# Performance work log

Measured on AMD Instinct MI355X. Metric: run time of the kernel, lower is better.

## Reference

```python
import jax, jax.numpy as jnp
import numpy as np

B, S, D = 32, 512, 512
H, DK, DV, DFF = 8, 64, 64, 2048
TEMP = float(np.sqrt(DK))  # d_k ** 0.5
COS_EPS = 1e-8             # torch.cosine_similarity eps
LN_EPS = 1e-5


def _layernorm(x, g, b):
    mu = jnp.mean(x, axis=-1, keepdims=True)
    var = jnp.var(x, axis=-1, keepdims=True)
    return (x - mu) * jax.lax.rsqrt(var + LN_EPS) * g + b


def setup_inputs() -> dict:
    key = jax.random.key(0)
    ks = jax.random.split(key, 12)
    s = 0.02
    return {
        "x": jax.random.normal(ks[0], (B, S, D), dtype=jnp.float32),
        "w_q": jax.random.normal(ks[1], (D, H * DK), dtype=jnp.float32) * s,
        "w_k": jax.random.normal(ks[2], (D, H * DK), dtype=jnp.float32) * s,
        "w_v": jax.random.normal(ks[3], (D, H * DV), dtype=jnp.float32) * s,
        "w_o": jax.random.normal(ks[4], (H * DV, D), dtype=jnp.float32) * s,
        "w_ff1": jax.random.normal(ks[5], (D, DFF), dtype=jnp.float32) * s,
        "b_ff1": jnp.zeros((DFF,), dtype=jnp.float32),
        "w_ff2": jax.random.normal(ks[6], (DFF, D), dtype=jnp.float32) * s,
        "b_ff2": jnp.zeros((D,), dtype=jnp.float32),
        "g1": jnp.ones((D,), dtype=jnp.float32),
        "b1": jnp.zeros((D,), dtype=jnp.float32),
        "g2": jnp.ones((D,), dtype=jnp.float32),
        "b2": jnp.zeros((D,), dtype=jnp.float32),
    }


def reference(x, w_q, w_k, w_v, w_o, w_ff1, b_ff1, w_ff2, b_ff2, g1, b1, g2, b2):
    b, s, _ = x.shape
    # projections -> [b, h, s, d]
    q = (x @ w_q).reshape(b, s, H, DK).transpose(0, 2, 1, 3)
    k = (x @ w_k).reshape(b, s, H, DK).transpose(0, 2, 1, 3)
    v = (x @ w_v).reshape(b, s, H, DV).transpose(0, 2, 1, 3)
    # cosine-similarity attention: dot(q,k) / max(||q||*||k||, eps) / temperature
    scores = jnp.einsum("bhqd,bhkd->bhqk", q, k)
    nq = jnp.linalg.norm(q, axis=-1)  # [b,h,s]
    nk = jnp.linalg.norm(k, axis=-1)
    denom = jnp.maximum(nq[:, :, :, None] * nk[:, :, None, :], COS_EPS)
    attn = jax.nn.softmax(scores / denom / TEMP, axis=-1)
    out = jnp.einsum("bhqk,bhkd->bhqd", attn, v)  # [b,h,s,dv]
    out = out.transpose(0, 2, 1, 3).reshape(b, s, H * DV) @ w_o
    # residual + LN1
    h1 = _layernorm(x + out, g1, b1)
    # FFN
    ffn = jax.nn.relu(h1 @ w_ff1 + b_ff1) @ w_ff2 + b_ff2
    # residual + LN2
    return _layernorm(h1 + ffn, g2, b2)
```

## Files before the change

### kernel.cpp

```cpp
#include <hip/hip_runtime.h>
#include <cmath>

typedef __bf16 bf16x8 __attribute__((ext_vector_type(8)));
typedef __bf16 bf16x4 __attribute__((ext_vector_type(4)));
typedef float  floatx4 __attribute__((ext_vector_type(4)));

#define LN_EPS 1e-5f
#define INV_TEMP 0.125f

static const int Mrows = 16384;

__device__ __forceinline__ void gload_lds16(const void* g, void* l) {
  __builtin_amdgcn_global_load_lds(
      (const __attribute__((address_space(1))) void*)g,
      (__attribute__((address_space(3))) void*)l, 16, 0, 0);
}

__global__ __launch_bounds__(256) void prep_kernel(const float* __restrict__ x, __bf16* __restrict__ xb,
                                                   const float* __restrict__ wq, const float* __restrict__ wk,
                                                   const float* __restrict__ wv, const float* __restrict__ wo,
                                                   const float* __restrict__ wff1, const float* __restrict__ wff2,
                                                   __bf16* __restrict__ tq, __bf16* __restrict__ tk,
                                                   __bf16* __restrict__ tv, __bf16* __restrict__ to_,
                                                   __bf16* __restrict__ tff1, __bf16* __restrict__ tff2) {
  const int bid = blockIdx.x, tid = threadIdx.x;
  if (bid < 8192) {
    int i = bid * 256 + tid;
    float4 v = ((const float4*)x)[i];
    __bf16* d = xb + i * 4;
    d[0] = (__bf16)v.x; d[1] = (__bf16)v.y; d[2] = (__bf16)v.z; d[3] = (__bf16)v.w;
    return;
  }
  __shared__ __bf16 til[64][72];
  int t = bid - 8192;
  const float* src; __bf16* dst; int R, C, bx, by;
  if (t < 256) {
    int w = t >> 6, tt = t & 63;
    const float* srcs[4] = {wq, wk, wv, wo};
    __bf16* dsts[4] = {tq, tk, tv, to_};
    src = srcs[w]; dst = dsts[w]; R = 512; C = 512; bx = tt & 7; by = tt >> 3;
  } else if (t < 512) {
    int tt = t - 256;
    src = wff1; dst = tff1; R = 512; C = 2048; bx = tt & 31; by = tt >> 5;
  } else {
    int tt = t - 512;
    src = wff2; dst = tff2; R = 2048; C = 512; bx = tt & 7; by = tt >> 3;
  }
  const float* s = src + (size_t)(by * 64) * C + bx * 64;
  int r = tid >> 4, c4 = (tid & 15) * 4;
  for (int p = 0; p < 4; ++p) {
    int rr = r + p * 16;
    float4 v = *(const float4*)(s + (size_t)rr * C + c4);
    til[c4 + 0][rr] = (__bf16)v.x;
    til[c4 + 1][rr] = (__bf16)v.y;
    til[c4 + 2][rr] = (__bf16)v.z;
    til[c4 + 3][rr] = (__bf16)v.w;
  }
  __syncthreads();
  __bf16* d = dst + (size_t)(bx * 64) * R + by * 64;
  int orow = tid >> 3, oc8 = (tid & 7) * 8;
  for (int p = 0; p < 2; ++p) {
    int rr = orow + p * 32;
    *(bf16x8*)(d + (size_t)rr * R + oc8) = *(const bf16x8*)(&til[rr][oc8]);
  }
}

template <int EPI, int NBN, int NDIM, int KDIM>
__global__ __launch_bounds__(256) void gemm_bt(const __bf16* __restrict__ A,
                                               const __bf16* __restrict__ Bt,
                                               __bf16* __restrict__ Cv,
                                               const float* __restrict__ bias,
                                               float* __restrict__ norms,
                                               __bf16* __restrict__ vtg) {
  __shared__ __align__(16) char smem[128 * 144 * 2];
  __bf16* As = (__bf16*)smem;
  __bf16* Bs = (__bf16*)(smem + 16384);
  const int tid = threadIdx.x;
  const int wave = tid >> 6, lane = tid & 63;
  const int l15 = lane & 15, quad = lane >> 4;
  const int id = blockIdx.x;
  const int xcd = id & 7, t = id >> 3;
  const int nblk = t % NBN, mblk = (t / NBN) * 8 + xcd;
  const int m0 = mblk * 128, n0 = nblk * 128;
  const int wrow = (wave >> 1) * 64, wcol = (wave & 1) * 64;
  const int rs = lane >> 3;
  const int swz_st = ((lane & 7) ^ rs) * 8;
  const int s7 = l15 & 7;

  floatx4 zero = {0.f, 0.f, 0.f, 0.f};
  floatx4 acc[4][4];
  for (int i = 0; i < 4; ++i)
    for (int j = 0; j < 4; ++j) acc[i][j] = zero;

  for (int kt = 0; kt < KDIM; kt += 64) {
    __syncthreads();
    for (int c = 0; c < 8; ++c) {
      int g = wave * 8 + c;
      const __bf16* src;
      __bf16* dst;
      if (g < 16) {
        int row = m0 + g * 8 + rs;
        src = A + (size_t)row * KDIM + kt + swz_st;
        dst = As + g * 512;
      } else {
        int g2 = g - 16;
        int row = n0 + g2 * 8 + rs;
        src = Bt + (size_t)row * KDIM + kt + swz_st;
        dst = Bs + g2 * 512;
      }
      gload_lds16(src, dst + lane * 8);
    }
    __syncthreads();
    for (int hh = 0; hh < 2; ++hh) {
      int ko = ((hh * 4 + quad) ^ s7) * 8;
      bf16x8 a[4], b[4];
      for (int i = 0; i < 4; ++i)
        a[i] = *(const bf16x8*)(As + (wrow + i * 16 + l15) * 64 + ko);
      for (int j = 0; j < 4; ++j)
        b[j] = *(const bf16x8*)(Bs + (wcol + j * 16 + l15) * 64 + ko);
      for (int i = 0; i < 4; ++i)
        for (int j = 0; j < 4; ++j)
          acc[i][j] = __builtin_amdgcn_mfma_f32_16x16x32_bf16(a[i], b[j], acc[i][j], 0, 0, 0);
    }
  }

  if (EPI == 4) {
    int head_global = (n0 + wcol) >> 6;
    int kind = head_global >> 3;
    if (kind < 2) {
      int h = head_global & 7;
      for (int i = 0; i < 4; ++i)
        for (int r = 0; r < 4; ++r) {
          float sq = 0.f;
          for (int j = 0; j < 4; ++j) {
            float v = acc[i][j][r];
            sq += v * v;
          }
          for (int m = 1; m < 16; m <<= 1) sq += __shfl_xor(sq, m, 64);
          if (l15 == 0) {
            int arow = m0 + wrow + i * 16 + quad * 4 + r;
            int bb = arow >> 9, ss = arow & 511;
            norms[kind * 131072 + ((bb << 3) + h) * 512 + ss] = rsqrtf(sq);
          }
        }
    } else {
      __syncthreads();
      __bf16* Ct = (__bf16*)smem;
      for (int i = 0; i < 4; ++i)
        for (int j = 0; j < 4; ++j) {
          bf16x4 pk;
          for (int r = 0; r < 4; ++r) pk[r] = (__bf16)acc[i][j][r];
          *(bf16x4*)(Ct + (wcol + j * 16 + l15) * 136 + wrow + i * 16 + quad * 4) = pk;
        }
      __syncthreads();
      int b = mblk >> 2, s0r = (mblk & 3) * 128;
      for (int p = 0; p < 8; ++p) {
        int row = p * 16 + (tid >> 4);
        int c8 = (tid & 15) * 8;
        int colg = n0 + row;
        int h = (colg >> 6) & 7, d = colg & 63;
        *(bf16x8*)(vtg + ((size_t)(((b << 3) + h) * 64 + d)) * 512 + s0r + c8) =
            *(const bf16x8*)(Ct + row * 136 + c8);
      }
      return;
    }
  }

  __syncthreads();
  __bf16* Cs = (__bf16*)smem;
  for (int i = 0; i < 4; ++i)
    for (int j = 0; j < 4; ++j) {
      int coll = wcol + j * 16 + l15;
      float bv = (EPI == 2) ? bias[n0 + coll] : 0.f;
      for (int r = 0; r < 4; ++r) {
        float v = acc[i][j][r];
        if (EPI == 2) {
          v += bv;
          v = v > 0.f ? v : 0.f;
        }
        Cs[(wrow + i * 16 + quad * 4 + r) * 144 + coll] = (__bf16)v;
      }
    }
  __syncthreads();
  for (int p = 0; p < 8; ++p) {
    int row = p * 16 + (tid >> 4);
    int c8 = (tid & 15) * 8;
    *(bf16x8*)(Cv + (size_t)(m0 + row) * NDIM + n0 + c8) =
        *(const bf16x8*)(Cs + row * 144 + c8);
  }
}

template <int EPI, int NBN, int NDIM, int KDIM, int NKS>
__global__ __launch_bounds__(512, 2) void gemm256(const __bf16* __restrict__ A,
                                                  const __bf16* __restrict__ Bt,
                                                  __bf16* __restrict__ Cv,
                                                  const float* __restrict__ bias) {
  __shared__ __align__(16) char smem[131072];
  const int tid = threadIdx.x;
  const int wave = tid >> 6, lane = tid & 63;
  const int l15 = lane & 15, quad = lane >> 4;
  const int wm = wave >> 2, wn = wave & 3;
  const int s7 = l15 & 7;
  const int rs = lane >> 3, slot = lane & 7;
  const int swz = (slot ^ rs) * 8;

  constexpr int NBM = Mrows / 256;
  constexpr int NBLK = NBM * NBN * NKS;
  constexpr int KS = KDIM / NKS;
  constexpr int NT = KS / 64;

  int id = blockIdx.x;
  int t = (id & 7) * (NBLK >> 3) + (id >> 3);
  const int ks = t / (NBM * NBN);
  t -= ks * (NBM * NBN);
  const int nblk = t % NBN, mblk = t / NBN;
  const int m0 = mblk * 256, n0 = nblk * 256;
  const __bf16* Ab = A + (size_t)ks * KS;
  const __bf16* Bb = Bt + (size_t)ks * KS;
  __bf16* Cw = Cv + (size_t)ks * Mrows * NDIM;
  (void)bias;

  const __bf16* sb[4][2];
  int ldo[4][2];
#pragma unroll
  for (int s = 0; s < 4; ++s)
#pragma unroll
    for (int j = 0; j < 2; ++j) {
      int chunk;
      if (s < 2) {
        int c = (wave & 3) * 4 + s * 2 + j;
        if (wave < 4) chunk = (c < 8) ? c : c + 8;
        else          chunk = 32 + ((c >> 2) * 8 + (c & 3));
      } else if (s == 2) {
        int c = 2 * wave + j;
        chunk = (c < 8) ? c + 8 : c + 16;
      } else {
        int c = 2 * wave + j;
        chunk = 32 + ((c >> 2) * 8 + 4 + (c & 3));
      }
      int isB = chunk >= 32 ? 1 : 0;
      int cc = chunk - isB * 32;
      int row = cc * 8 + rs;
      sb[s][j] = (isB ? (Bb + (size_t)(n0 + row) * KDIM)
                      : (Ab + (size_t)(m0 + row) * KDIM)) + swz;
      ldo[s][j] = isB * 32768 + cc * 1024 + lane * 16;
    }

  floatx4 zero = {0.f, 0.f, 0.f, 0.f};
  floatx4 acc[8][4];
#pragma unroll
  for (int i = 0; i < 8; ++i)
#pragma unroll
    for (int j = 0; j < 4; ++j) acc[i][j] = zero;

#define STAGE256(s, ktel, bufb)                                              \
  {                                                                          \
    gload_lds16(sb[s][0] + (ktel), smem + (bufb) * 65536 + ldo[s][0]);       \
    gload_lds16(sb[s][1] + (ktel), smem + (bufb) * 65536 + ldo[s][1]);       \
  }

#define PHASE256(q, ia, jb, bufb, DOSTAGE, ktel)                                   \
  {                                                                                \
    const __bf16* Abuf = (const __bf16*)(smem + (bufb) * 65536);                   \
    const __bf16* Bbuf = Abuf + 16384;                                             \
    bf16x8 af[4][2], bfr[2][2];                                                    \
    _Pragma("unroll") for (int i = 0; i < 4; ++i) {                                \
      int row = wm * 128 + (ia) * 64 + i * 16 + l15;                               \
      af[i][0] = *(const bf16x8*)(Abuf + row * 64 + ((quad ^ s7) * 8));            \
      af[i][1] = *(const bf16x8*)(Abuf + row * 64 + (((4 + quad) ^ s7) * 8));      \
    }                                                                              \
    _Pragma("unroll") for (int j = 0; j < 2; ++j) {                                \
      int row = wn * 64 + (jb) * 32 + j * 16 + l15;                                \
      bfr[j][0] = *(const bf16x8*)(Bbuf + row * 64 + ((quad ^ s7) * 8));           \
      bfr[j][1] = *(const bf16x8*)(Bbuf + row * 64 + (((4 + quad) ^ s7) * 8));     \
    }                                                                              \
    if (DOSTAGE) STAGE256(q, ktel, (bufb) ^ 1);                                    \
    __builtin_amdgcn_s_barrier();                                                  \
    asm volatile("s_waitcnt lgkmcnt(0)" ::: "memory");                             \
    __builtin_amdgcn_s_setprio(1);                                                 \
    _Pragma("unroll") for (int i = 0; i < 4; ++i)                                  \
      _Pragma("unroll") for (int j = 0; j < 2; ++j) {                              \
        acc[(ia) * 4 + i][(jb) * 2 + j] = __builtin_amdgcn_mfma_f32_16x16x32_bf16( \
            af[i][0], bfr[j][0], acc[(ia) * 4 + i][(jb) * 2 + j], 0, 0, 0);        \
        acc[(ia) * 4 + i][(jb) * 2 + j] = __builtin_amdgcn_mfma_f32_16x16x32_bf16( \
            af[i][1], bfr[j][1], acc[(ia) * 4 + i][(jb) * 2 + j], 0, 0, 0);        \
      }                                                                            \
    __builtin_amdgcn_s_setprio(0);                                                 \
    asm volatile("s_waitcnt vmcnt(4)" ::: "memory");                               \
    __builtin_amdgcn_s_barrier();                                                  \
  }

#pragma unroll
  for (int s = 0; s < 4; ++s) STAGE256(s, 0, 0);
  asm volatile("s_waitcnt vmcnt(0)" ::: "memory");
  __builtin_amdgcn_s_barrier();

  for (int t2 = 0; t2 < NT - 1; ++t2) {
    int b = t2 & 1;
    int k1 = (t2 + 1) * 64;
    PHASE256(0, 0, 0, b, 1, k1);
    PHASE256(1, 1, 0, b, 1, k1);
    PHASE256(2, 1, 1, b, 1, k1);
    PHASE256(3, 0, 1, b, 1, k1);
  }
  asm volatile("s_waitcnt vmcnt(0)" ::: "memory");
  __builtin_amdgcn_s_barrier();
  {
    const int b = (NT - 1) & 1;
    PHASE256(0, 0, 0, b, 0, 0);
    PHASE256(1, 1, 0, b, 0, 0);
    PHASE256(2, 1, 1, b, 0, 0);
    PHASE256(3, 0, 1, b, 0, 0);
  }

  const int PADC = 264;
  __bf16* Cs = (__bf16*)smem;
  float bv[4];
  if (EPI == 2) {
#pragma unroll
    for (int j = 0; j < 4; ++j) bv[j] = bias[n0 + wn * 64 + j * 16 + l15];
  }
#pragma unroll
  for (int hh = 0; hh < 2; ++hh) {
    __builtin_amdgcn_s_barrier();
    if (wm == hh) {
#pragma unroll
      for (int i = 0; i < 8; ++i)
#pragma unroll
        for (int j = 0; j < 4; ++j)
#pragma unroll
          for (int r = 0; r < 4; ++r) {
            float v = acc[i][j][r];
            if (EPI == 2) {
              v += bv[j];
              v = v > 0.f ? v : 0.f;
            }
            Cs[(i * 16 + quad * 4 + r) * PADC + wn * 64 + j * 16 + l15] = (__bf16)v;
          }
    }
    __builtin_amdgcn_s_barrier();
#pragma unroll
    for (int p = 0; p < 8; ++p) {
      int rowl = p * 16 + (tid >> 5);
      int c8 = (tid & 31) * 8;
      *(bf16x8*)(Cw + (size_t)(m0 + hh * 128 + rowl) * NDIM + n0 + c8) =
          *(const bf16x8*)(Cs + rowl * PADC + c8);
    }
  }
#undef STAGE256
#undef PHASE256
}

__global__ __launch_bounds__(256) void attn_kernel(const __bf16* __restrict__ qkv,
                                                   const __bf16* __restrict__ vtg,
                                                   const float* __restrict__ norms,
                                                   __bf16* __restrict__ out) {
  __shared__ __align__(16) __bf16 Ks[64 * 64];
  __shared__ __align__(16) __bf16 Vs[64 * 64];
  __shared__ __align__(16) __bf16 P2[4][16 * 72];
  const int tid = threadIdx.x, wave = tid >> 6, lane = tid & 63;
  const int l15 = lane & 15, quad = lane >> 4;
  const int bh = blockIdx.x & 255;
  const int qq = blockIdx.x >> 8;
  const int b = bh >> 3, h = bh & 7;
  const int qbase = qq * 128 + wave * 32;
  const int rs = lane >> 3;
  const int swz_st = ((lane & 7) ^ rs) * 8;
  const int s7 = l15 & 7;

  const __bf16* Qb = qkv + (size_t)(b * 512) * 1536 + h * 64;
  const __bf16* Kb = Qb + 512;
  const __bf16* Vtb = vtg + (size_t)bh * 32768;
  const float* nkinv = norms + 131072 + bh * 512;
  const float* nqinv = norms + bh * 512;
  __bf16* Pw = P2[wave];

  bf16x8 aq[2][2];
  float cq[2];
  for (int ch = 0; ch < 2; ++ch) {
    int qrow = qbase + ch * 16;
    aq[ch][0] = *(const bf16x8*)(Qb + (size_t)(qrow + l15) * 1536 + quad * 8);
    aq[ch][1] = *(const bf16x8*)(Qb + (size_t)(qrow + l15) * 1536 + 32 + quad * 8);
    cq[ch] = nqinv[qrow + l15] * INV_TEMP;
  }

  floatx4 zero = {0.f, 0.f, 0.f, 0.f};
  floatx4 o[2][4];
  float lsum[2] = {0.f, 0.f};
  for (int ch = 0; ch < 2; ++ch)
    for (int jd = 0; jd < 4; ++jd) o[ch][jd] = zero;

  for (int kt = 0; kt < 8; ++kt) {
    int s0 = kt * 64;
    __syncthreads();
    for (int c = 0; c < 4; ++c) {
      int g = wave * 4 + c;
      const __bf16* src;
      __bf16* dst;
      if (g < 8) {
        int sk = g * 8 + rs;
        src = Kb + (size_t)(s0 + sk) * 1536 + swz_st;
        dst = Ks + g * 512;
      } else {
        int g2 = g - 8;
        int d = g2 * 8 + rs;
        src = Vtb + (size_t)d * 512 + s0 + swz_st;
        dst = Vs + g2 * 512;
      }
      gload_lds16(src, dst + lane * 8);
    }
    __syncthreads();

    for (int ch = 0; ch < 2; ++ch) {
      floatx4 z[4];
      for (int j = 0; j < 4; ++j) {
        int r64 = (j * 16 + l15) * 64;
        bf16x8 k0 = *(const bf16x8*)(Ks + r64 + ((quad ^ s7) * 8));
        bf16x8 k1 = *(const bf16x8*)(Ks + r64 + (((4 + quad) ^ s7) * 8));
        floatx4 zz = zero;
        zz = __builtin_amdgcn_mfma_f32_16x16x32_bf16(k0, aq[ch][0], zz, 0, 0, 0);
        zz = __builtin_amdgcn_mfma_f32_16x16x32_bf16(k1, aq[ch][1], zz, 0, 0, 0);
        z[j] = zz;
      }
      for (int j = 0; j < 4; ++j) {
        floatx4 nk4 = *(const floatx4*)(nkinv + s0 + j * 16 + quad * 4);
        bf16x4 pk;
        for (int r = 0; r < 4; ++r) {
          float p = __expf(z[j][r] * cq[ch] * nk4[r]);
          lsum[ch] += p;
          pk[r] = (__bf16)p;
        }
        *(bf16x4*)(Pw + l15 * 72 + j * 16 + quad * 4) = pk;
      }
      bf16x8 ap0 = *(const bf16x8*)(Pw + l15 * 72 + quad * 8);
      bf16x8 ap1 = *(const bf16x8*)(Pw + l15 * 72 + 32 + quad * 8);
      for (int jd = 0; jd < 4; ++jd) {
        int r64 = (jd * 16 + l15) * 64;
        bf16x8 v0 = *(const bf16x8*)(Vs + r64 + ((quad ^ s7) * 8));
        bf16x8 v1 = *(const bf16x8*)(Vs + r64 + (((4 + quad) ^ s7) * 8));
        o[ch][jd] = __builtin_amdgcn_mfma_f32_16x16x32_bf16(v0, ap0, o[ch][jd], 0, 0, 0);
        o[ch][jd] = __builtin_amdgcn_mfma_f32_16x16x32_bf16(v1, ap1, o[ch][jd], 0, 0, 0);
      }
    }
  }

  for (int ch = 0; ch < 2; ++ch) {
    float s = lsum[ch];
    s += __shfl_xor(s, 16, 64);
    s += __shfl_xor(s, 32, 64);
    float inv = __builtin_amdgcn_rcpf(s);
    int q = qbase + ch * 16 + l15;
    __bf16* op = out + (size_t)(b * 512 + q) * 512 + h * 64;
    for (int jd = 0; jd < 4; ++jd) {
      bf16x4 pk;
      for (int r = 0; r < 4; ++r) pk[r] = (__bf16)(o[ch][jd][r] * inv);
      *(bf16x4*)(op + jd * 16 + quad * 4) = pk;
    }
  }
}

template <bool X1BF, bool WF, bool WB, bool DUAL>
__global__ __launch_bounds__(256) void resid_ln(const float* __restrict__ X1f,
                                                const __bf16* __restrict__ X1b,
                                                const __bf16* __restrict__ X2,
                                                const __bf16* __restrict__ X2b,
                                                const float* __restrict__ bias,
                                                const float* __restrict__ g,
                                                const float* __restrict__ be,
                                                float* __restrict__ outf,
                                                __bf16* __restrict__ outb) {
  int row = blockIdx.x * 4 + (threadIdx.x >> 6);
  int lane = threadIdx.x & 63;
  float v[8];
  bf16x8 b8 = *(const bf16x8*)(X2 + (size_t)row * 512 + lane * 8);
  if (X1BF) {
    bf16x8 a = *(const bf16x8*)(X1b + (size_t)row * 512 + lane * 8);
    for (int i = 0; i < 8; ++i) v[i] = (float)a[i] + (float)b8[i];
  } else {
    const float4* r1 = (const float4*)(X1f + (size_t)row * 512);
    float4 a0 = r1[lane * 2], a1 = r1[lane * 2 + 1];
    v[0] = a0.x; v[1] = a0.y; v[2] = a0.z; v[3] = a0.w;
    v[4] = a1.x; v[5] = a1.y; v[6] = a1.z; v[7] = a1.w;
    for (int i = 0; i < 8; ++i) v[i] += (float)b8[i];
  }
  if (DUAL) {
    bf16x8 c8 = *(const bf16x8*)(X2b + (size_t)row * 512 + lane * 8);
    for (int i = 0; i < 8; ++i) v[i] += (float)c8[i];
  }
  if (bias) {
    const float* bp = bias + lane * 8;
    for (int i = 0; i < 8; ++i) v[i] += bp[i];
  }
  float s = 0.f, sq = 0.f;
  for (int i = 0; i < 8; ++i) {
    s += v[i];
    sq += v[i] * v[i];
  }
  for (int m = 1; m < 64; m <<= 1) {
    s += __shfl_xor(s, m, 64);
    sq += __shfl_xor(sq, m, 64);
  }
  float mean = s * (1.f / 512.f);
  float var = sq * (1.f / 512.f) - mean * mean;
  float rstd = rsqrtf(var + LN_EPS);
  const float* gp = g + lane * 8;
  const float* bp2 = be + lane * 8;
  float o[8];
  for (int i = 0; i < 8; ++i) o[i] = (v[i] - mean) * rstd * gp[i] + bp2[i];
  if (WF) {
    float4 w0 = {o[0], o[1], o[2], o[3]}, w1 = {o[4], o[5], o[6], o[7]};
    ((float4*)(outf + (size_t)row * 512))[lane * 2] = w0;
    ((float4*)(outf + (size_t)row * 512))[lane * 2 + 1] = w1;
  }
  if (WB) {
    __bf16 tmp[8];
    for (int i = 0; i < 8; ++i) tmp[i] = (__bf16)o[i];
    *(bf16x8*)(outb + (size_t)row * 512 + lane * 8) = *(bf16x8*)tmp;
  }
}

extern "C" void kernel_launch(void* const* d_in, const int* in_sizes, int n_in,
                              void* d_out, int out_size, void* d_ws, size_t ws_size,
                              hipStream_t stream) {
  const float* x     = (const float*)d_in[0];
  const float* w_q   = (const float*)d_in[1];
  const float* w_k   = (const float*)d_in[2];
  const float* w_v   = (const float*)d_in[3];
  const float* w_o   = (const float*)d_in[4];
  const float* w_ff1 = (const float*)d_in[5];
  const float* b_ff1 = (const float*)d_in[6];
  const float* w_ff2 = (const float*)d_in[7];
  const float* b_ff2 = (const float*)d_in[8];
  const float* g1    = (const float*)d_in[9];
  const float* b1    = (const float*)d_in[10];
  const float* g2    = (const float*)d_in[11];
  const float* b2    = (const float*)d_in[12];
  float* out = (float*)d_out;

  char* ws = (char*)d_ws;
  size_t off = 0;
  auto alloc = [&](size_t bytes) -> void* {
    void* p = ws + off;
    off += (bytes + 255) & ~(size_t)255;
    return p;
  };
  __bf16* xb     = (__bf16*)alloc((size_t)Mrows * 512 * 2);
  __bf16* wt_qkv = (__bf16*)alloc((size_t)1536 * 512 * 2);
  __bf16* wt_o   = (__bf16*)alloc((size_t)512 * 512 * 2);
  __bf16* wt_ff1 = (__bf16*)alloc((size_t)2048 * 512 * 2);
  __bf16* wt_ff2 = (__bf16*)alloc((size_t)512 * 2048 * 2);
  __bf16* qkv    = (__bf16*)alloc((size_t)Mrows * 1536 * 2);
  float*  norms  = (float*)alloc((size_t)262144 * 4);
  __bf16* attn   = (__bf16*)alloc((size_t)Mrows * 512 * 2);
  __bf16* projb  = (__bf16*)alloc((size_t)Mrows * 512 * 2);
  __bf16* h1b    = (__bf16*)alloc((size_t)Mrows * 512 * 2);
  __bf16* mid    = (__bf16*)alloc((size_t)Mrows * 2048 * 2);
  __bf16* vtg    = mid;
  __bf16* f2o    = attn;

  prep_kernel<<<8960, 256, 0, stream>>>(x, xb, w_q, w_k, w_v, w_o, w_ff1, w_ff2,
                                        wt_qkv, wt_qkv + 512 * 512, wt_qkv + 2 * 512 * 512,
                                        wt_o, wt_ff1, wt_ff2);

  gemm_bt<4, 12, 1536, 512><<<dim3(12 * 128), 256, 0, stream>>>(xb, wt_qkv, qkv, nullptr,
                                                                norms, vtg);
  attn_kernel<<<dim3(1024), 256, 0, stream>>>(qkv, vtg, norms, attn);
  gemm_bt<0, 4, 512, 512><<<dim3(4 * 128), 256, 0, stream>>>(attn, wt_o, projb, nullptr,
                                                             nullptr, nullptr);
  resid_ln<false, false, true, false><<<4096, 256, 0, stream>>>(x, nullptr, projb, nullptr,
                                                                nullptr, g1, b1, nullptr, h1b);
  gemm256<2, 8, 2048, 512, 1><<<dim3(512), 512, 0, stream>>>(h1b, wt_ff1, mid, b_ff1);
  gemm256<0, 2, 512, 2048, 2><<<dim3(256), 512, 0, stream>>>(mid, wt_ff2, f2o, nullptr);
  resid_ln<true, true, false, true><<<4096, 256, 0, stream>>>(nullptr, h1b, f2o,
                                                              f2o + (size_t)Mrows * 512,
                                                              b_ff2, g2, b2, out, nullptr);
}
```

Before: 320.9 us.

## Move QKV projection to 256x256 gemm with fused norm/V-transpose epilogue and reworked pipeline

The QKV projection now runs on the 256x256-tile, 512-thread gemm256 kernel instead of the 128-tile gemm_bt. The norm and V-transpose epilogue is moved into gemm256 so the larger tile still produces the cosine norms and the transposed V. The gemm256 main loop is also restructured: each wave stages contiguous rows, and a k-tile is split into four MFMA quadrants with A/B fragment loads interleaved between barriers. This aims for more reuse per block and better overlap of LDS reads with MFMA. The cost is more barriers per k-tile and a full vmcnt(0) wait at the end of each tile, and the changes also affect the FF1 and FF2 gemms.

```diff
diff --git a/kernel.cpp b/kernel.cpp
--- a/kernel.cpp
+++ b/kernel.cpp
@@ -124,48 +124,6 @@
     }
   }
 
-  if (EPI == 4) {
-    int head_global = (n0 + wcol) >> 6;
-    int kind = head_global >> 3;
-    if (kind < 2) {
-      int h = head_global & 7;
-      for (int i = 0; i < 4; ++i)
-        for (int r = 0; r < 4; ++r) {
-          float sq = 0.f;
-          for (int j = 0; j < 4; ++j) {
-            float v = acc[i][j][r];
-            sq += v * v;
-          }
-          for (int m = 1; m < 16; m <<= 1) sq += __shfl_xor(sq, m, 64);
-          if (l15 == 0) {
-            int arow = m0 + wrow + i * 16 + quad * 4 + r;
-            int bb = arow >> 9, ss = arow & 511;
-            norms[kind * 131072 + ((bb << 3) + h) * 512 + ss] = rsqrtf(sq);
-          }
-        }
-    } else {
-      __syncthreads();
-      __bf16* Ct = (__bf16*)smem;
-      for (int i = 0; i < 4; ++i)
-        for (int j = 0; j < 4; ++j) {
-          bf16x4 pk;
-          for (int r = 0; r < 4; ++r) pk[r] = (__bf16)acc[i][j][r];
-          *(bf16x4*)(Ct + (wcol + j * 16 + l15) * 136 + wrow + i * 16 + quad * 4) = pk;
-        }
-      __syncthreads();
-      int b = mblk >> 2, s0r = (mblk & 3) * 128;
-      for (int p = 0; p < 8; ++p) {
-        int row = p * 16 + (tid >> 4);
-        int c8 = (tid & 15) * 8;
-        int colg = n0 + row;
-        int h = (colg >> 6) & 7, d = colg & 63;
-        *(bf16x8*)(vtg + ((size_t)(((b << 3) + h) * 64 + d)) * 512 + s0r + c8) =
-            *(const bf16x8*)(Ct + row * 136 + c8);
-      }
-      return;
-    }
-  }
-
   __syncthreads();
   __bf16* Cs = (__bf16*)smem;
   for (int i = 0; i < 4; ++i)
@@ -194,7 +152,9 @@
 __global__ __launch_bounds__(512, 2) void gemm256(const __bf16* __restrict__ A,
                                                   const __bf16* __restrict__ Bt,
                                                   __bf16* __restrict__ Cv,
-                                                  const float* __restrict__ bias) {
+                                                  const float* __restrict__ bias,
+                                                  float* __restrict__ norms,
+                                                  __bf16* __restrict__ vtg) {
   __shared__ __align__(16) char smem[131072];
   const int tid = threadIdx.x;
   const int wave = tid >> 6, lane = tid & 63;
@@ -220,31 +180,12 @@
   __bf16* Cw = Cv + (size_t)ks * Mrows * NDIM;
   (void)bias;
 
-  const __bf16* sb[4][2];
-  int ldo[4][2];
-#pragma unroll
-  for (int s = 0; s < 4; ++s)
-#pragma unroll
-    for (int j = 0; j < 2; ++j) {
-      int chunk;
-      if (s < 2) {
-        int c = (wave & 3) * 4 + s * 2 + j;
-        if (wave < 4) chunk = (c < 8) ? c : c + 8;
-        else          chunk = 32 + ((c >> 2) * 8 + (c & 3));
-      } else if (s == 2) {
-        int c = 2 * wave + j;
-        chunk = (c < 8) ? c + 8 : c + 16;
-      } else {
-        int c = 2 * wave + j;
-        chunk = 32 + ((c >> 2) * 8 + 4 + (c & 3));
-      }
-      int isB = chunk >= 32 ? 1 : 0;
-      int cc = chunk - isB * 32;
-      int row = cc * 8 + rs;
-      sb[s][j] = (isB ? (Bb + (size_t)(n0 + row) * KDIM)
-                      : (Ab + (size_t)(m0 + row) * KDIM)) + swz;
-      ldo[s][j] = isB * 32768 + cc * 1024 + lane * 16;
-    }
+  const int isB = wave >= 4 ? 1 : 0;
+  const int w3 = wave & 3;
+  const __bf16* sbase = isB
+      ? Bb + (size_t)(n0 + w3 * 64 + rs) * KDIM + swz
+      : Ab + (size_t)(m0 + w3 * 64 + rs) * KDIM + swz;
+  const int ldob = isB * 32768 + w3 * 8192 + lane * 16;
 
   floatx4 zero = {0.f, 0.f, 0.f, 0.f};
   floatx4 acc[8][4];
@@ -253,64 +194,145 @@
 #pragma unroll
     for (int j = 0; j < 4; ++j) acc[i][j] = zero;
 
-#define STAGE256(s, ktel, bufb)                                              \
-  {                                                                          \
-    gload_lds16(sb[s][0] + (ktel), smem + (bufb) * 65536 + ldo[s][0]);       \
-    gload_lds16(sb[s][1] + (ktel), smem + (bufb) * 65536 + ldo[s][1]);       \
-  }
-
-#define PHASE256(q, ia, jb, bufb, DOSTAGE, ktel)                                   \
+  bf16x8 aR[4][2];
+  bf16x8 bC[2][2][2];
+
+#define STAGE8(jj, ktel, bufb)                                             \
+  gload_lds16(sbase + (size_t)(jj) * (8 * KDIM) + (ktel),                  \
+              smem + (bufb) * 65536 + ldob + (jj) * 1024);
+
+#define LDA256(ia, bufb)                                                        \
+  {                                                                             \
+    const __bf16* Abuf = (const __bf16*)(smem + (size_t)(bufb) * 65536);        \
+    _Pragma("unroll") for (int i = 0; i < 4; ++i) {                             \
+      int row = wm * 128 + (ia) * 64 + i * 16 + l15;                            \
+      aR[i][0] = *(const bf16x8*)(Abuf + row * 64 + ((quad ^ s7) * 8));         \
+      aR[i][1] = *(const bf16x8*)(Abuf + row * 64 + (((4 + quad) ^ s7) * 8));   \
+    }                                                                           \
+  }
+
+#define LDB256(jb, bufb)                                                              \
+  {                                                                                   \
+    const __bf16* Bbuf = (const __bf16*)(smem + (size_t)(bufb) * 65536) + 16384;      \
+    _Pragma("unroll") for (int j = 0; j < 2; ++j) {                                   \
+      int row = wn * 64 + (jb) * 32 + j * 16 + l15;                                   \
+      bC[jb][j][0] = *(const bf16x8*)(Bbuf + row * 64 + ((quad ^ s7) * 8));           \
+      bC[jb][j][1] = *(const bf16x8*)(Bbuf + row * 64 + (((4 + quad) ^ s7) * 8));     \
+    }                                                                                 \
+  }
+
+#define MFMAQ(ia, jb)                                                              \
   {                                                                                \
-    const __bf16* Abuf = (const __bf16*)(smem + (bufb) * 65536);                   \
-    const __bf16* Bbuf = Abuf + 16384;                                             \
-    bf16x8 af[4][2], bfr[2][2];                                                    \
-    _Pragma("unroll") for (int i = 0; i < 4; ++i) {                                \
-      int row = wm * 128 + (ia) * 64 + i * 16 + l15;                               \
-      af[i][0] = *(const bf16x8*)(Abuf + row * 64 + ((quad ^ s7) * 8));            \
-      af[i][1] = *(const bf16x8*)(Abuf + row * 64 + (((4 + quad) ^ s7) * 8));      \
-    }                                                                              \
-    _Pragma("unroll") for (int j = 0; j < 2; ++j) {                                \
-      int row = wn * 64 + (jb) * 32 + j * 16 + l15;                                \
-      bfr[j][0] = *(const bf16x8*)(Bbuf + row * 64 + ((quad ^ s7) * 8));           \
-      bfr[j][1] = *(const bf16x8*)(Bbuf + row * 64 + (((4 + quad) ^ s7) * 8));     \
-    }                                                                              \
-    if (DOSTAGE) STAGE256(q, ktel, (bufb) ^ 1);                                    \
-    __builtin_amdgcn_s_barrier();                                                  \
-    asm volatile("s_waitcnt lgkmcnt(0)" ::: "memory");                             \
     __builtin_amdgcn_s_setprio(1);                                                 \
     _Pragma("unroll") for (int i = 0; i < 4; ++i)                                  \
       _Pragma("unroll") for (int j = 0; j < 2; ++j) {                              \
         acc[(ia) * 4 + i][(jb) * 2 + j] = __builtin_amdgcn_mfma_f32_16x16x32_bf16( \
-            af[i][0], bfr[j][0], acc[(ia) * 4 + i][(jb) * 2 + j], 0, 0, 0);        \
+            aR[i][0], bC[jb][j][0], acc[(ia) * 4 + i][(jb) * 2 + j], 0, 0, 0);     \
         acc[(ia) * 4 + i][(jb) * 2 + j] = __builtin_amdgcn_mfma_f32_16x16x32_bf16( \
-            af[i][1], bfr[j][1], acc[(ia) * 4 + i][(jb) * 2 + j], 0, 0, 0);        \
+            aR[i][1], bC[jb][j][1], acc[(ia) * 4 + i][(jb) * 2 + j], 0, 0, 0);     \
       }                                                                            \
     __builtin_amdgcn_s_setprio(0);                                                 \
-    asm volatile("s_waitcnt vmcnt(4)" ::: "memory");                               \
-    __builtin_amdgcn_s_barrier();                                                  \
-  }
-
-#pragma unroll
-  for (int s = 0; s < 4; ++s) STAGE256(s, 0, 0);
+  }
+
+#define KTILE(bufb, DOSTAGE, ktel)                                         \
+  {                                                                        \
+    LDA256(0, bufb);                                                       \
+    LDB256(0, bufb);                                                       \
+    if (DOSTAGE) {                                                         \
+      STAGE8(0, ktel, (bufb) ^ 1); STAGE8(1, ktel, (bufb) ^ 1);            \
+      STAGE8(2, ktel, (bufb) ^ 1); STAGE8(3, ktel, (bufb) ^ 1);            \
+    }                                                                      \
+    __builtin_amdgcn_s_barrier();                                          \
+    asm volatile("s_waitcnt lgkmcnt(0)" ::: "memory");                     \
+    MFMAQ(0, 0);                                                           \
+    __builtin_amdgcn_s_barrier();                                          \
+    LDB256(1, bufb);                                                       \
+    if (DOSTAGE) {                                                         \
+      STAGE8(4, ktel, (bufb) ^ 1); STAGE8(5, ktel, (bufb) ^ 1);            \
+      STAGE8(6, ktel, (bufb) ^ 1); STAGE8(7, ktel, (bufb) ^ 1);            \
+    }                                                                      \
+    __builtin_amdgcn_s_barrier();                                          \
+    asm volatile("s_waitcnt lgkmcnt(0)" ::: "memory");                     \
+    MFMAQ(0, 1);                                                           \
+    __builtin_amdgcn_s_barrier();                                          \
+    LDA256(1, bufb);                                                       \
+    __builtin_amdgcn_s_barrier();                                          \
+    asm volatile("s_waitcnt lgkmcnt(0)" ::: "memory");                     \
+    MFMAQ(1, 1);                                                           \
+    __builtin_amdgcn_s_barrier();                                          \
+    MFMAQ(1, 0);                                                           \
+    if (DOSTAGE) asm volatile("s_waitcnt vmcnt(0)" ::: "memory");          \
+    __builtin_amdgcn_s_barrier();                                          \
+  }
+
+#pragma unroll
+  for (int jj = 0; jj < 8; ++jj) STAGE8(jj, 0, 0);
   asm volatile("s_waitcnt vmcnt(0)" ::: "memory");
   __builtin_amdgcn_s_barrier();
 
   for (int t2 = 0; t2 < NT - 1; ++t2) {
-    int b = t2 & 1;
-    int k1 = (t2 + 1) * 64;
-    PHASE256(0, 0, 0, b, 1, k1);
-    PHASE256(1, 1, 0, b, 1, k1);
-    PHASE256(2, 1, 1, b, 1, k1);
-    PHASE256(3, 0, 1, b, 1, k1);
-  }
-  asm volatile("s_waitcnt vmcnt(0)" ::: "memory");
-  __builtin_amdgcn_s_barrier();
-  {
-    const int b = (NT - 1) & 1;
-    PHASE256(0, 0, 0, b, 0, 0);
-    PHASE256(1, 1, 0, b, 0, 0);
-    PHASE256(2, 1, 1, b, 0, 0);
-    PHASE256(3, 0, 1, b, 0, 0);
+    KTILE(t2 & 1, 1, (t2 + 1) * 64);
+  }
+  KTILE((NT - 1) & 1, 0, 0);
+
+#undef STAGE8
+#undef LDA256
+#undef LDB256
+#undef MFMAQ
+#undef KTILE
+
+  if (EPI == 4) {
+    int head_global = (n0 + wn * 64) >> 6;
+    int kind = head_global >> 3;
+    if (kind < 2) {
+      int h = head_global & 7;
+#pragma unroll
+      for (int ii = 0; ii < 8; ++ii)
+#pragma unroll
+        for (int r = 0; r < 4; ++r) {
+          float sq = 0.f;
+#pragma unroll
+          for (int jj = 0; jj < 4; ++jj) {
+            float v = acc[ii][jj][r];
+            sq += v * v;
+          }
+          for (int m = 1; m < 16; m <<= 1) sq += __shfl_xor(sq, m, 64);
+          if (l15 == 0) {
+            int arow = m0 + wm * 128 + ii * 16 + quad * 4 + r;
+            int bb = arow >> 9, ss = arow & 511;
+            norms[kind * 131072 + ((bb << 3) + h) * 512 + ss] = rsqrtf(sq);
+          }
+        }
+    } else {
+      const int PADT = 136;
+      __bf16* Ct = (__bf16*)smem;
+      int bb = m0 >> 9, s0r = m0 & 511;
+#pragma unroll
+      for (int hh = 0; hh < 2; ++hh) {
+        __builtin_amdgcn_s_barrier();
+        if (wm == hh) {
+#pragma unroll
+          for (int ii = 0; ii < 8; ++ii)
+#pragma unroll
+            for (int jj = 0; jj < 4; ++jj) {
+              bf16x4 pk;
+#pragma unroll
+              for (int r = 0; r < 4; ++r) pk[r] = (__bf16)acc[ii][jj][r];
+              *(bf16x4*)(Ct + (wn * 64 + jj * 16 + l15) * PADT + ii * 16 + quad * 4) = pk;
+            }
+        }
+        __builtin_amdgcn_s_barrier();
+#pragma unroll
+        for (int p = 0; p < 8; ++p) {
+          int c = p * 32 + (tid >> 4);
+          int s8 = (tid & 15) * 8;
+          int h = ((n0 + c) >> 6) & 7, d = c & 63;
+          *(bf16x8*)(vtg + ((size_t)(((bb << 3) + h) * 64 + d)) * 512 + s0r + hh * 128 + s8) =
+              *(const bf16x8*)(Ct + c * PADT + s8);
+        }
+      }
+      return;
+    }
   }
 
   const int PADC = 264;
@@ -347,8 +369,6 @@
           *(const bf16x8*)(Cs + rowl * PADC + c8);
     }
   }
-#undef STAGE256
-#undef PHASE256
 }
 
 __global__ __launch_bounds__(256) void attn_kernel(const __bf16* __restrict__ qkv,
@@ -562,15 +582,17 @@
                                         wt_qkv, wt_qkv + 512 * 512, wt_qkv + 2 * 512 * 512,
                                         wt_o, wt_ff1, wt_ff2);
 
-  gemm_bt<4, 12, 1536, 512><<<dim3(12 * 128), 256, 0, stream>>>(xb, wt_qkv, qkv, nullptr,
-                                                                norms, vtg);
+  gemm256<4, 6, 1536, 512, 1><<<dim3(384), 512, 0, stream>>>(xb, wt_qkv, qkv, nullptr,
+                                                             norms, vtg);
   attn_kernel<<<dim3(1024), 256, 0, stream>>>(qkv, vtg, norms, attn);
   gemm_bt<0, 4, 512, 512><<<dim3(4 * 128), 256, 0, stream>>>(attn, wt_o, projb, nullptr,
                                                              nullptr, nullptr);
   resid_ln<false, false, true, false><<<4096, 256, 0, stream>>>(x, nullptr, projb, nullptr,
                                                                 nullptr, g1, b1, nullptr, h1b);
-  gemm256<2, 8, 2048, 512, 1><<<dim3(512), 512, 0, stream>>>(h1b, wt_ff1, mid, b_ff1);
-  gemm256<0, 2, 512, 2048, 2><<<dim3(256), 512, 0, stream>>>(mid, wt_ff2, f2o, nullptr);
+  gemm256<2, 8, 2048, 512, 1><<<dim3(512), 512, 0, stream>>>(h1b, wt_ff1, mid, b_ff1,
+                                                             nullptr, nullptr);
+  gemm256<0, 2, 512, 2048, 2><<<dim3(256), 512, 0, stream>>>(mid, wt_ff2, f2o, nullptr,
+                                                             nullptr, nullptr);
   resid_ln<true, true, false, true><<<4096, 256, 0, stream>>>(nullptr, h1b, f2o,
                                                               f2o + (size_t)Mrows * 512,
                                                               b_ff2, g2, b2, out, nullptr);
```

Measured after the change: 321.9 us. Within noise of the previous version (+0.3%).
